# Kernel tuning notes

Measured on AMD Instinct MI355X. Metric: run time of the kernel, lower is better.

## Reference

```python
import jax, jax.numpy as jnp
import numpy as np

N_NODES = 50000
N_EDGES = 800000
D_IN = 128
D_HID = 256
N_CLASSES = 2
N_GRAPHS = 256


def _graph_conv(x, src, dst, W_root, W_rel, b, num_nodes):
    # PyG GraphConv: out_i = W_root @ x_i + W_rel @ sum_{j->i} x_j + b
    agg = jax.ops.segment_sum(x[src], dst, num_segments=num_nodes)  # [N, d_in]
    return x @ W_root.T + agg @ W_rel.T + b


def setup_inputs() -> dict:
    key = jax.random.key(0)
    ks = jax.random.split(key, 12)
    x = jax.random.normal(ks[0], (N_NODES, D_IN), dtype=jnp.float32)
    edge_index = jax.random.randint(ks[1], (2, N_EDGES), 0, N_NODES, dtype=jnp.int64)
    batch = jnp.sort(jax.random.randint(ks[2], (N_NODES,), 0, N_GRAPHS, dtype=jnp.int64))
    s1 = 1.0 / np.sqrt(D_IN)
    s2 = 1.0 / np.sqrt(D_HID)
    W1_root = jax.random.uniform(ks[3], (D_HID, D_IN), minval=-s1, maxval=s1, dtype=jnp.float32)
    W1_rel = jax.random.uniform(ks[4], (D_HID, D_IN), minval=-s1, maxval=s1, dtype=jnp.float32)
    b1 = jax.random.uniform(ks[5], (D_HID,), minval=-s1, maxval=s1, dtype=jnp.float32)
    W2_root = jax.random.uniform(ks[6], (D_HID, D_HID), minval=-s2, maxval=s2, dtype=jnp.float32)
    W2_rel = jax.random.uniform(ks[7], (D_HID, D_HID), minval=-s2, maxval=s2, dtype=jnp.float32)
    b2 = jax.random.uniform(ks[8], (D_HID,), minval=-s2, maxval=s2, dtype=jnp.float32)
    Wfc = jax.random.uniform(ks[9], (N_CLASSES, D_HID), minval=-s2, maxval=s2, dtype=jnp.float32)
    bfc = jax.random.uniform(ks[10], (N_CLASSES,), minval=-s2, maxval=s2, dtype=jnp.float32)
    return {"x": x, "edge_index": edge_index, "batch": batch, "num_graphs": N_GRAPHS,
            "W1_root": W1_root, "W1_rel": W1_rel, "b1": b1,
            "W2_root": W2_root, "W2_rel": W2_rel, "b2": b2,
            "Wfc": Wfc, "bfc": bfc}


def reference(x, edge_index, batch, num_graphs, W1_root, W1_rel, b1, W2_root, W2_rel, b2, Wfc, bfc):
    src, dst = edge_index[0], edge_index[1]
    n = x.shape[0]
    h = jax.nn.relu(_graph_conv(x, src, dst, W1_root, W1_rel, b1, n))
    h = jax.nn.relu(_graph_conv(h, src, dst, W2_root, W2_rel, b2, n))
    # global mean pool over graph segments
    sums = jax.ops.segment_sum(h, batch, num_segments=num_graphs)        # [G, d]
    counts = jax.ops.segment_sum(jnp.ones((n,), h.dtype), batch, num_segments=num_graphs)
    pooled = sums / jnp.maximum(counts, 1.0)[:, None]
    logits = pooled @ Wfc.T + bfc
    return jax.nn.sigmoid(logits)
```

## Files before the change

### kernel.cpp

```cpp
#include <hip/hip_runtime.h>
#include <math.h>

#define D_IN 128
#define D_HID 256
#define N_CLASSES 2
#define N_GRAPHS 256
#define BUCKET 64

typedef __attribute__((ext_vector_type(8))) short short8;
typedef __attribute__((ext_vector_type(4))) float float4v;

__device__ __forceinline__ unsigned short f2bf(float f) {
    union { float f; unsigned int u; } v; v.f = f;
    unsigned int r = v.u + 0x7FFFu + ((v.u >> 16) & 1u);
    return (unsigned short)(r >> 16);
}
__device__ __forceinline__ float bf2f(unsigned short h) {
    union { unsigned int u; float f; } v; v.u = ((unsigned int)h) << 16;
    return v.f;
}

#define GLD_LDS16(gp, lp) __builtin_amdgcn_global_load_lds( \
    (const __attribute__((address_space(1))) void*)(gp),    \
    (__attribute__((address_space(3))) void*)(lp), 16, 0, 0)

__global__ void convert_all_kernel(const float* __restrict__ x,
                                   const float* __restrict__ w1r,
                                   const float* __restrict__ w1a,
                                   const float* __restrict__ w2r,
                                   const float* __restrict__ w2a,
                                   unsigned short* __restrict__ xb,
                                   unsigned short* __restrict__ o1r,
                                   unsigned short* __restrict__ o1a,
                                   unsigned short* __restrict__ o2r,
                                   unsigned short* __restrict__ o2a,
                                   int n4x) {
    int i = blockIdx.x * blockDim.x + threadIdx.x;
    const float* in; unsigned short* out; int off;
    if (i < n4x)                 { in = x;   out = xb;  off = i; }
    else {
        int j = i - n4x;
        if (j < 8192)            { in = w1r; out = o1r; off = j; }
        else if (j < 16384)      { in = w1a; out = o1a; off = j - 8192; }
        else if (j < 32768)      { in = w2r; out = o2r; off = j - 16384; }
        else if (j < 49152)      { in = w2a; out = o2a; off = j - 32768; }
        else return;
    }
    float4 v = ((const float4*)in)[off];
    ushort4 o;
    o.x = f2bf(v.x); o.y = f2bf(v.y); o.z = f2bf(v.z); o.w = f2bf(v.w);
    ((ushort4*)out)[off] = o;
}

__global__ void fill_bucket_kernel(const int* __restrict__ src, const int* __restrict__ dst,
                                   int* __restrict__ cursor, unsigned short* __restrict__ srcs,
                                   int E) {
    int e = blockIdx.x * blockDim.x + threadIdx.x;
    if (e < E) {
        int d = dst[e];
        int pos = atomicAdd(&cursor[d], 1);
        if (pos < BUCKET) srcs[d * BUCKET + pos] = (unsigned short)src[e];
    }
}

template <int D>
__global__ void gather_bucket_bf16(const unsigned short* __restrict__ feat,
                                   const unsigned short* __restrict__ srcs,
                                   const int* __restrict__ cnt,
                                   unsigned short* __restrict__ agg, int N) {
    const int wave = (blockIdx.x * blockDim.x + threadIdx.x) >> 6;
    const int lane = threadIdx.x & 63;
    if (wave >= N) return;
    const unsigned short* bucket = srcs + (size_t)wave * BUCKET;
    int my = bucket[lane];
    const int c = min(cnt[wave], BUCKET);

    if (D == 256) {
        float a0 = 0.f, a1 = 0.f, a2 = 0.f, a3 = 0.f;
        float b0 = 0.f, b1 = 0.f, b2 = 0.f, b3 = 0.f;
        const unsigned short* base = feat + lane * 4;
        int i = 0;
        for (; i + 4 <= c; i += 4) {
            int s0 = __shfl(my, i + 0);
            int s1 = __shfl(my, i + 1);
            int s2 = __shfl(my, i + 2);
            int s3 = __shfl(my, i + 3);
            uint2 w0 = *(const uint2*)(base + (size_t)s0 * 256);
            uint2 w1 = *(const uint2*)(base + (size_t)s1 * 256);
            uint2 w2 = *(const uint2*)(base + (size_t)s2 * 256);
            uint2 w3 = *(const uint2*)(base + (size_t)s3 * 256);
            a0 += bf2f((unsigned short)(w0.x & 0xFFFF)); a1 += bf2f((unsigned short)(w0.x >> 16));
            a2 += bf2f((unsigned short)(w0.y & 0xFFFF)); a3 += bf2f((unsigned short)(w0.y >> 16));
            b0 += bf2f((unsigned short)(w1.x & 0xFFFF)); b1 += bf2f((unsigned short)(w1.x >> 16));
            b2 += bf2f((unsigned short)(w1.y & 0xFFFF)); b3 += bf2f((unsigned short)(w1.y >> 16));
            a0 += bf2f((unsigned short)(w2.x & 0xFFFF)); a1 += bf2f((unsigned short)(w2.x >> 16));
            a2 += bf2f((unsigned short)(w2.y & 0xFFFF)); a3 += bf2f((unsigned short)(w2.y >> 16));
            b0 += bf2f((unsigned short)(w3.x & 0xFFFF)); b1 += bf2f((unsigned short)(w3.x >> 16));
            b2 += bf2f((unsigned short)(w3.y & 0xFFFF)); b3 += bf2f((unsigned short)(w3.y >> 16));
        }
        for (; i < c; i++) {
            int s = __shfl(my, i);
            uint2 w = *(const uint2*)(base + (size_t)s * 256);
            a0 += bf2f((unsigned short)(w.x & 0xFFFF)); a1 += bf2f((unsigned short)(w.x >> 16));
            a2 += bf2f((unsigned short)(w.y & 0xFFFF)); a3 += bf2f((unsigned short)(w.y >> 16));
        }
        a0 += b0; a1 += b1; a2 += b2; a3 += b3;
        uint2 o;
        o.x = (unsigned int)f2bf(a0) | ((unsigned int)f2bf(a1) << 16);
        o.y = (unsigned int)f2bf(a2) | ((unsigned int)f2bf(a3) << 16);
        *(uint2*)(agg + (size_t)wave * 256 + lane * 4) = o;
    } else {
        const int half = lane >> 5;
        const int hl = lane & 31;
        float a0 = 0.f, a1 = 0.f, a2 = 0.f, a3 = 0.f;
        float b0 = 0.f, b1 = 0.f, b2 = 0.f, b3 = 0.f;
        const unsigned short* base = feat + hl * 4;
        int i = 0;
        for (; i + 4 <= c; i += 4) {
            int sA = __shfl(my, i + half);
            int sB = __shfl(my, i + 2 + half);
            uint2 wA = *(const uint2*)(base + (size_t)sA * 128);
            uint2 wB = *(const uint2*)(base + (size_t)sB * 128);
            a0 += bf2f((unsigned short)(wA.x & 0xFFFF)); a1 += bf2f((unsigned short)(wA.x >> 16));
            a2 += bf2f((unsigned short)(wA.y & 0xFFFF)); a3 += bf2f((unsigned short)(wA.y >> 16));
            b0 += bf2f((unsigned short)(wB.x & 0xFFFF)); b1 += bf2f((unsigned short)(wB.x >> 16));
            b2 += bf2f((unsigned short)(wB.y & 0xFFFF)); b3 += bf2f((unsigned short)(wB.y >> 16));
        }
        for (; i < c; i += 2) {
            if (i + half < c) {
                int s = __shfl(my, i + half);
                uint2 w = *(const uint2*)(base + (size_t)s * 128);
                a0 += bf2f((unsigned short)(w.x & 0xFFFF)); a1 += bf2f((unsigned short)(w.x >> 16));
                a2 += bf2f((unsigned short)(w.y & 0xFFFF)); a3 += bf2f((unsigned short)(w.y >> 16));
            }
        }
        a0 += b0; a1 += b1; a2 += b2; a3 += b3;
        a0 += __shfl_xor(a0, 32);
        a1 += __shfl_xor(a1, 32);
        a2 += __shfl_xor(a2, 32);
        a3 += __shfl_xor(a3, 32);
        if (half == 0) {
            uint2 o;
            o.x = (unsigned int)f2bf(a0) | ((unsigned int)f2bf(a1) << 16);
            o.y = (unsigned int)f2bf(a2) | ((unsigned int)f2bf(a3) << 16);
            *(uint2*)(agg + (size_t)wave * 128 + hl * 4) = o;
        }
    }
}

template <int K1>
__global__ void gemm_mfma_dual(const unsigned short* __restrict__ X,
                               const unsigned short* __restrict__ Ag,
                               const unsigned short* __restrict__ Wr,
                               const unsigned short* __restrict__ Wa,
                               const float* __restrict__ bias,
                               unsigned short* __restrict__ out,
                               int Nrows) {
    __shared__ __align__(16) unsigned short As[128][32];
    __shared__ __align__(16) unsigned short Bs[128][32];

    const int tid = threadIdx.x;
    const int w = tid >> 6;
    const int lane = tid & 63;
    const int quad = lane >> 4;
    const int r16 = lane & 15;
    const int srow = lane >> 2;
    const int scol = (lane & 3) * 8;
    const int i0 = blockIdx.x * 128;
    const int o0 = blockIdx.y * 128;
    const int m0 = (w >> 1) * 64;
    const int n0 = (w & 1) * 64;

    float4v acc[4][4];
#pragma unroll
    for (int mt = 0; mt < 4; mt++)
#pragma unroll
        for (int nt = 0; nt < 4; nt++) {
            float4v z = {0.f, 0.f, 0.f, 0.f};
            acc[mt][nt] = z;
        }

    for (int k0 = 0; k0 < 2 * K1; k0 += 32) {
        const bool first = (k0 < K1);
        const int kb = first ? k0 : (k0 - K1);
        const unsigned short* PA = first ? X : Ag;
        const unsigned short* PB = first ? Wr : Wa;

#pragma unroll
        for (int t = 0; t < 2; t++) {
            const int rr = w * 32 + t * 16;
            GLD_LDS16(PA + (size_t)(i0 + rr + srow) * K1 + kb + scol, &As[rr][0]);
            GLD_LDS16(PB + (size_t)(o0 + rr + srow) * K1 + kb + scol, &Bs[rr][0]);
        }
        __syncthreads();

        short8 af[4], bfr[4];
#pragma unroll
        for (int mt = 0; mt < 4; mt++)
            af[mt] = *(const short8*)&As[m0 + mt * 16 + r16][quad * 8];
#pragma unroll
        for (int nt = 0; nt < 4; nt++)
            bfr[nt] = *(const short8*)&Bs[n0 + nt * 16 + r16][quad * 8];
#pragma unroll
        for (int mt = 0; mt < 4; mt++)
#pragma unroll
            for (int nt = 0; nt < 4; nt++)
                acc[mt][nt] = __builtin_amdgcn_mfma_f32_16x16x32_bf16(
                    af[mt], bfr[nt], acc[mt][nt], 0, 0, 0);
        __syncthreads();
    }

#pragma unroll
    for (int mt = 0; mt < 4; mt++) {
#pragma unroll
        for (int e = 0; e < 4; e++) {
            const int m = i0 + m0 + mt * 16 + quad * 4 + e;
            if (m >= Nrows) continue;
#pragma unroll
            for (int nt = 0; nt < 4; nt++) {
                const int n = o0 + n0 + nt * 16 + r16;
                float v = acc[mt][nt][e] + bias[n];
                out[(size_t)m * 256 + n] = f2bf(fmaxf(v, 0.f));
            }
        }
    }
}

__global__ void pool_fc_kernel(const unsigned short* __restrict__ h,
                               const int* __restrict__ batch,
                               const float* __restrict__ Wfc,
                               const float* __restrict__ bfc,
                               float* __restrict__ out,
                               int N) {
    const int g = blockIdx.x;
    const int tid = threadIdx.x;
    const int wv = tid >> 6;
    const int lane = tid & 63;

    int lo = 0, hi = N;
    while (lo < hi) { int mid = (lo + hi) >> 1; if (batch[mid] < g) lo = mid + 1; else hi = mid; }
    const int start = lo;
    hi = N;
    while (lo < hi) { int mid = (lo + hi) >> 1; if (batch[mid] < g + 1) lo = mid + 1; else hi = mid; }
    const int end = lo;

    float a0 = 0.f, a1 = 0.f, a2 = 0.f, a3 = 0.f;
    float b0 = 0.f, b1 = 0.f, b2 = 0.f, b3 = 0.f;
    const unsigned short* base = h + lane * 4;
    int r = start + wv;
    for (; r + 16 < end; r += 32) {
        uint2 wA = *(const uint2*)(base + (size_t)r * 256);
        uint2 wB = *(const uint2*)(base + (size_t)(r + 16) * 256);
        a0 += bf2f((unsigned short)(wA.x & 0xFFFF)); a1 += bf2f((unsigned short)(wA.x >> 16));
        a2 += bf2f((unsigned short)(wA.y & 0xFFFF)); a3 += bf2f((unsigned short)(wA.y >> 16));
        b0 += bf2f((unsigned short)(wB.x & 0xFFFF)); b1 += bf2f((unsigned short)(wB.x >> 16));
        b2 += bf2f((unsigned short)(wB.y & 0xFFFF)); b3 += bf2f((unsigned short)(wB.y >> 16));
    }
    if (r < end) {
        uint2 wA = *(const uint2*)(base + (size_t)r * 256);
        a0 += bf2f((unsigned short)(wA.x & 0xFFFF)); a1 += bf2f((unsigned short)(wA.x >> 16));
        a2 += bf2f((unsigned short)(wA.y & 0xFFFF)); a3 += bf2f((unsigned short)(wA.y >> 16));
    }
    a0 += b0; a1 += b1; a2 += b2; a3 += b3;

    __shared__ float part[16][D_HID];
    part[wv][lane * 4 + 0] = a0;
    part[wv][lane * 4 + 1] = a1;
    part[wv][lane * 4 + 2] = a2;
    part[wv][lane * 4 + 3] = a3;
    __syncthreads();

    __shared__ float pooled[D_HID];
    __shared__ float red[2 * D_HID];
    if (tid < D_HID) {
        float s = 0.f;
#pragma unroll
        for (int w2 = 0; w2 < 16; w2++) s += part[w2][tid];
        const float cnt = fmaxf((float)(end - start), 1.0f);
        pooled[tid] = s / cnt;
    }
    __syncthreads();

    if (tid < 2 * D_HID) {
        const int c = tid >> 8;
        const int col = tid & 255;
        red[tid] = pooled[col] * Wfc[c * D_HID + col];
    }
    __syncthreads();
    for (int off = D_HID / 2; off > 0; off >>= 1) {
        if (tid < 2 * D_HID && (tid & 255) < off) red[tid] += red[tid + off];
        __syncthreads();
    }
    if (tid < N_CLASSES) {
        float logit = red[tid << 8] + bfc[tid];
        out[g * N_CLASSES + tid] = 1.0f / (1.0f + expf(-logit));
    }
}

extern "C" void kernel_launch(void* const* d_in, const int* in_sizes, int n_in,
                              void* d_out, int out_size, void* d_ws, size_t ws_size,
                              hipStream_t stream) {
    const float* x     = (const float*)d_in[0];
    const int*   edge  = (const int*)d_in[1];
    const int*   batch = (const int*)d_in[2];
    const float* W1r = (const float*)d_in[4];
    const float* W1a = (const float*)d_in[5];
    const float* b1  = (const float*)d_in[6];
    const float* W2r = (const float*)d_in[7];
    const float* W2a = (const float*)d_in[8];
    const float* b2  = (const float*)d_in[9];
    const float* Wfc = (const float*)d_in[10];
    const float* bfc = (const float*)d_in[11];

    const int N = in_sizes[0] / D_IN;
    const int E = in_sizes[1] / 2;
    const int* src = edge;
    const int* dst = edge + E;

    unsigned short* xb    = (unsigned short*)d_ws;
    unsigned short* agg1b = xb    + (size_t)N * 128;
    unsigned short* h1b   = agg1b + (size_t)N * 128;
    unsigned short* agg2b = h1b   + (size_t)N * 256;
    unsigned short* h2b   = agg2b + (size_t)N * 256;
    unsigned short* w1r_b = h2b   + (size_t)N * 256;
    unsigned short* w1a_b = w1r_b + 256 * 128;
    unsigned short* w2r_b = w1a_b + 256 * 128;
    unsigned short* w2a_b = w2r_b + 256 * 256;
    int* cursor = (int*)(w2a_b + 256 * 256);
    unsigned short* srcs = (unsigned short*)(cursor + N);

    hipMemsetAsync(cursor, 0, (size_t)N * sizeof(int), stream);

    {
        int n4x = N * D_IN / 4;
        int total = n4x + 49152;
        convert_all_kernel<<<(total + 255) / 256, 256, 0, stream>>>(
            x, W1r, W1a, W2r, W2a, xb, w1r_b, w1a_b, w2r_b, w2a_b, n4x);
    }

    fill_bucket_kernel<<<(E + 255) / 256, 256, 0, stream>>>(src, dst, cursor, srcs, E);

    gather_bucket_bf16<D_IN><<<(N + 3) / 4, 256, 0, stream>>>(xb, srcs, cursor, agg1b, N);
    {
        dim3 grid((N + 127) / 128, 2);
        gemm_mfma_dual<D_IN><<<grid, 256, 0, stream>>>(
            xb, agg1b, w1r_b, w1a_b, b1, h1b, N);
    }

    gather_bucket_bf16<D_HID><<<(N + 3) / 4, 256, 0, stream>>>(h1b, srcs, cursor, agg2b, N);
    {
        dim3 grid((N + 127) / 128, 2);
        gemm_mfma_dual<D_HID><<<grid, 256, 0, stream>>>(
            h1b, agg2b, w2r_b, w2a_b, b2, h2b, N);
    }

    pool_fc_kernel<<<N_GRAPHS, 1024, 0, stream>>>(h2b, batch, Wfc, bfc, (float*)d_out, N);
}
```

Before: 280.3 us.

## Pad neighbor buckets to multiples of 8 with a zero row, fuse convert and fill

```diff
diff --git a/kernel.cpp b/kernel.cpp
--- a/kernel.cpp
+++ b/kernel.cpp
@@ -19,48 +19,73 @@
     union { unsigned int u; float f; } v; v.u = ((unsigned int)h) << 16;
     return v.f;
 }
+__device__ __forceinline__ float blo(unsigned int u) {
+    union { unsigned int u; float f; } v; v.u = u << 16; return v.f;
+}
+__device__ __forceinline__ float bhi(unsigned int u) {
+    union { unsigned int u; float f; } v; v.u = u & 0xFFFF0000u; return v.f;
+}
 
 #define GLD_LDS16(gp, lp) __builtin_amdgcn_global_load_lds( \
     (const __attribute__((address_space(1))) void*)(gp),    \
     (__attribute__((address_space(3))) void*)(lp), 16, 0, 0)
 
-__global__ void convert_all_kernel(const float* __restrict__ x,
-                                   const float* __restrict__ w1r,
-                                   const float* __restrict__ w1a,
-                                   const float* __restrict__ w2r,
-                                   const float* __restrict__ w2a,
-                                   unsigned short* __restrict__ xb,
-                                   unsigned short* __restrict__ o1r,
-                                   unsigned short* __restrict__ o1a,
-                                   unsigned short* __restrict__ o2r,
-                                   unsigned short* __restrict__ o2a,
-                                   int n4x) {
-    int i = blockIdx.x * blockDim.x + threadIdx.x;
-    const float* in; unsigned short* out; int off;
-    if (i < n4x)                 { in = x;   out = xb;  off = i; }
-    else {
-        int j = i - n4x;
-        if (j < 8192)            { in = w1r; out = o1r; off = j; }
-        else if (j < 16384)      { in = w1a; out = o1a; off = j - 8192; }
-        else if (j < 32768)      { in = w2r; out = o2r; off = j - 16384; }
-        else if (j < 49152)      { in = w2a; out = o2a; off = j - 32768; }
-        else return;
-    }
-    float4 v = ((const float4*)in)[off];
-    ushort4 o;
-    o.x = f2bf(v.x); o.y = f2bf(v.y); o.z = f2bf(v.z); o.w = f2bf(v.w);
-    ((ushort4*)out)[off] = o;
-}
-
-__global__ void fill_bucket_kernel(const int* __restrict__ src, const int* __restrict__ dst,
-                                   int* __restrict__ cursor, unsigned short* __restrict__ srcs,
-                                   int E) {
-    int e = blockIdx.x * blockDim.x + threadIdx.x;
-    if (e < E) {
-        int d = dst[e];
-        int pos = atomicAdd(&cursor[d], 1);
-        if (pos < BUCKET) srcs[d * BUCKET + pos] = (unsigned short)src[e];
-    }
+__global__ void convert_fill_kernel(const float* __restrict__ x,
+                                    const float* __restrict__ w1r,
+                                    const float* __restrict__ w1a,
+                                    const float* __restrict__ w2r,
+                                    const float* __restrict__ w2a,
+                                    unsigned short* __restrict__ xb,
+                                    unsigned short* __restrict__ o1r,
+                                    unsigned short* __restrict__ o1a,
+                                    unsigned short* __restrict__ o2r,
+                                    unsigned short* __restrict__ o2a,
+                                    int n4x,
+                                    const int* __restrict__ src,
+                                    const int* __restrict__ dst,
+                                    int* __restrict__ cursor,
+                                    unsigned short* __restrict__ srcs,
+                                    int E, int convBlocks) {
+    if ((int)blockIdx.x < convBlocks) {
+        int i = blockIdx.x * blockDim.x + threadIdx.x;
+        const float* in; unsigned short* out; int off;
+        if (i < n4x)            { in = x;   out = xb;  off = i; }
+        else {
+            int j = i - n4x;
+            if (j < 8192)       { in = w1r; out = o1r; off = j; }
+            else if (j < 16384) { in = w1a; out = o1a; off = j - 8192; }
+            else if (j < 32768) { in = w2r; out = o2r; off = j - 16384; }
+            else if (j < 49152) { in = w2a; out = o2a; off = j - 32768; }
+            else return;
+        }
+        float4 v = ((const float4*)in)[off];
+        ushort4 o;
+        o.x = f2bf(v.x); o.y = f2bf(v.y); o.z = f2bf(v.z); o.w = f2bf(v.w);
+        ((ushort4*)out)[off] = o;
+    } else {
+        int e = ((int)blockIdx.x - convBlocks) * blockDim.x + threadIdx.x;
+        if (e < E) {
+            int d = dst[e];
+            int pos = atomicAdd(&cursor[d], 1);
+            if (pos < BUCKET) srcs[d * BUCKET + pos] = (unsigned short)src[e];
+        }
+    }
+}
+
+__global__ void pad_bucket_kernel(const int* __restrict__ cursor,
+                                  unsigned short* __restrict__ srcs,
+                                  unsigned short* __restrict__ xb_rowN,
+                                  unsigned short* __restrict__ h1b_rowN,
+                                  int N) {
+    if (blockIdx.x == 0) {
+        if (threadIdx.x < 64)  ((unsigned int*)xb_rowN)[threadIdx.x] = 0;
+        if (threadIdx.x < 128) ((unsigned int*)h1b_rowN)[threadIdx.x] = 0;
+    }
+    int n = blockIdx.x * blockDim.x + threadIdx.x;
+    if (n >= N) return;
+    int c = min(cursor[n], BUCKET);
+    int cpad = (c + 7) & ~7;
+    for (int i = c; i < cpad; i++) srcs[n * BUCKET + i] = (unsigned short)N;
 }
 
 template <int D>
@@ -74,35 +99,37 @@
     const unsigned short* bucket = srcs + (size_t)wave * BUCKET;
     int my = bucket[lane];
     const int c = min(cnt[wave], BUCKET);
+    const int cpad = (c + 7) & ~7;
 
     if (D == 256) {
         float a0 = 0.f, a1 = 0.f, a2 = 0.f, a3 = 0.f;
         float b0 = 0.f, b1 = 0.f, b2 = 0.f, b3 = 0.f;
         const unsigned short* base = feat + lane * 4;
-        int i = 0;
-        for (; i + 4 <= c; i += 4) {
+        for (int i = 0; i < cpad; i += 8) {
             int s0 = __shfl(my, i + 0);
             int s1 = __shfl(my, i + 1);
             int s2 = __shfl(my, i + 2);
             int s3 = __shfl(my, i + 3);
+            int s4 = __shfl(my, i + 4);
+            int s5 = __shfl(my, i + 5);
+            int s6 = __shfl(my, i + 6);
+            int s7 = __shfl(my, i + 7);
             uint2 w0 = *(const uint2*)(base + (size_t)s0 * 256);
             uint2 w1 = *(const uint2*)(base + (size_t)s1 * 256);
             uint2 w2 = *(const uint2*)(base + (size_t)s2 * 256);
             uint2 w3 = *(const uint2*)(base + (size_t)s3 * 256);
-            a0 += bf2f((unsigned short)(w0.x & 0xFFFF)); a1 += bf2f((unsigned short)(w0.x >> 16));
-            a2 += bf2f((unsigned short)(w0.y & 0xFFFF)); a3 += bf2f((unsigned short)(w0.y >> 16));
-            b0 += bf2f((unsigned short)(w1.x & 0xFFFF)); b1 += bf2f((unsigned short)(w1.x >> 16));
-            b2 += bf2f((unsigned short)(w1.y & 0xFFFF)); b3 += bf2f((unsigned short)(w1.y >> 16));
-            a0 += bf2f((unsigned short)(w2.x & 0xFFFF)); a1 += bf2f((unsigned short)(w2.x >> 16));
-            a2 += bf2f((unsigned short)(w2.y & 0xFFFF)); a3 += bf2f((unsigned short)(w2.y >> 16));
-            b0 += bf2f((unsigned short)(w3.x & 0xFFFF)); b1 += bf2f((unsigned short)(w3.x >> 16));
-            b2 += bf2f((unsigned short)(w3.y & 0xFFFF)); b3 += bf2f((unsigned short)(w3.y >> 16));
-        }
-        for (; i < c; i++) {
-            int s = __shfl(my, i);
-            uint2 w = *(const uint2*)(base + (size_t)s * 256);
-            a0 += bf2f((unsigned short)(w.x & 0xFFFF)); a1 += bf2f((unsigned short)(w.x >> 16));
-            a2 += bf2f((unsigned short)(w.y & 0xFFFF)); a3 += bf2f((unsigned short)(w.y >> 16));
+            uint2 w4 = *(const uint2*)(base + (size_t)s4 * 256);
+            uint2 w5 = *(const uint2*)(base + (size_t)s5 * 256);
+            uint2 w6 = *(const uint2*)(base + (size_t)s6 * 256);
+            uint2 w7 = *(const uint2*)(base + (size_t)s7 * 256);
+            a0 += blo(w0.x); a1 += bhi(w0.x); a2 += blo(w0.y); a3 += bhi(w0.y);
+            b0 += blo(w1.x); b1 += bhi(w1.x); b2 += blo(w1.y); b3 += bhi(w1.y);
+            a0 += blo(w2.x); a1 += bhi(w2.x); a2 += blo(w2.y); a3 += bhi(w2.y);
+            b0 += blo(w3.x); b1 += bhi(w3.x); b2 += blo(w3.y); b3 += bhi(w3.y);
+            a0 += blo(w4.x); a1 += bhi(w4.x); a2 += blo(w4.y); a3 += bhi(w4.y);
+            b0 += blo(w5.x); b1 += bhi(w5.x); b2 += blo(w5.y); b3 += bhi(w5.y);
+            a0 += blo(w6.x); a1 += bhi(w6.x); a2 += blo(w6.y); a3 += bhi(w6.y);
+            b0 += blo(w7.x); b1 += bhi(w7.x); b2 += blo(w7.y); b3 += bhi(w7.y);
         }
         a0 += b0; a1 += b1; a2 += b2; a3 += b3;
         uint2 o;
@@ -115,24 +142,19 @@
         float a0 = 0.f, a1 = 0.f, a2 = 0.f, a3 = 0.f;
         float b0 = 0.f, b1 = 0.f, b2 = 0.f, b3 = 0.f;
         const unsigned short* base = feat + hl * 4;
-        int i = 0;
-        for (; i + 4 <= c; i += 4) {
-            int sA = __shfl(my, i + half);
+        for (int i = 0; i < cpad; i += 8) {
+            int sA = __shfl(my, i + 0 + half);
             int sB = __shfl(my, i + 2 + half);
+            int sC = __shfl(my, i + 4 + half);
+            int sD = __shfl(my, i + 6 + half);
             uint2 wA = *(const uint2*)(base + (size_t)sA * 128);
             uint2 wB = *(const uint2*)(base + (size_t)sB * 128);
-            a0 += bf2f((unsigned short)(wA.x & 0xFFFF)); a1 += bf2f((unsigned short)(wA.x >> 16));
-            a2 += bf2f((unsigned short)(wA.y & 0xFFFF)); a3 += bf2f((unsigned short)(wA.y >> 16));
-            b0 += bf2f((unsigned short)(wB.x & 0xFFFF)); b1 += bf2f((unsigned short)(wB.x >> 16));
-            b2 += bf2f((unsigned short)(wB.y & 0xFFFF)); b3 += bf2f((unsigned short)(wB.y >> 16));
-        }
-        for (; i < c; i += 2) {
-            if (i + half < c) {
-                int s = __shfl(my, i + half);
-                uint2 w = *(const uint2*)(base + (size_t)s * 128);
-                a0 += bf2f((unsigned short)(w.x & 0xFFFF)); a1 += bf2f((unsigned short)(w.x >> 16));
-                a2 += bf2f((unsigned short)(w.y & 0xFFFF)); a3 += bf2f((unsigned short)(w.y >> 16));
-            }
+            uint2 wC = *(const uint2*)(base + (size_t)sC * 128);
+            uint2 wD = *(const uint2*)(base + (size_t)sD * 128);
+            a0 += blo(wA.x); a1 += bhi(wA.x); a2 += blo(wA.y); a3 += bhi(wA.y);
+            b0 += blo(wB.x); b1 += bhi(wB.x); b2 += blo(wB.y); b3 += bhi(wB.y);
+            a0 += blo(wC.x); a1 += bhi(wC.x); a2 += blo(wC.y); a3 += bhi(wC.y);
+            b0 += blo(wD.x); b1 += bhi(wD.x); b2 += blo(wD.y); b3 += bhi(wD.y);
         }
         a0 += b0; a1 += b1; a2 += b2; a3 += b3;
         a0 += __shfl_xor(a0, 32);
@@ -251,15 +273,12 @@
     for (; r + 16 < end; r += 32) {
         uint2 wA = *(const uint2*)(base + (size_t)r * 256);
         uint2 wB = *(const uint2*)(base + (size_t)(r + 16) * 256);
-        a0 += bf2f((unsigned short)(wA.x & 0xFFFF)); a1 += bf2f((unsigned short)(wA.x >> 16));
-        a2 += bf2f((unsigned short)(wA.y & 0xFFFF)); a3 += bf2f((unsigned short)(wA.y >> 16));
-        b0 += bf2f((unsigned short)(wB.x & 0xFFFF)); b1 += bf2f((unsigned short)(wB.x >> 16));
-        b2 += bf2f((unsigned short)(wB.y & 0xFFFF)); b3 += bf2f((unsigned short)(wB.y >> 16));
+        a0 += blo(wA.x); a1 += bhi(wA.x); a2 += blo(wA.y); a3 += bhi(wA.y);
+        b0 += blo(wB.x); b1 += bhi(wB.x); b2 += blo(wB.y); b3 += bhi(wB.y);
     }
     if (r < end) {
         uint2 wA = *(const uint2*)(base + (size_t)r * 256);
-        a0 += bf2f((unsigned short)(wA.x & 0xFFFF)); a1 += bf2f((unsigned short)(wA.x >> 16));
-        a2 += bf2f((unsigned short)(wA.y & 0xFFFF)); a3 += bf2f((unsigned short)(wA.y >> 16));
+        a0 += blo(wA.x); a1 += bhi(wA.x); a2 += blo(wA.y); a3 += bhi(wA.y);
     }
     a0 += b0; a1 += b1; a2 += b2; a3 += b3;
 
@@ -318,9 +337,9 @@
     const int* dst = edge + E;
 
     unsigned short* xb    = (unsigned short*)d_ws;
-    unsigned short* agg1b = xb    + (size_t)N * 128;
+    unsigned short* agg1b = xb    + (size_t)(N + 1) * 128;
     unsigned short* h1b   = agg1b + (size_t)N * 128;
-    unsigned short* agg2b = h1b   + (size_t)N * 256;
+    unsigned short* agg2b = h1b   + (size_t)(N + 1) * 256;
     unsigned short* h2b   = agg2b + (size_t)N * 256;
     unsigned short* w1r_b = h2b   + (size_t)N * 256;
     unsigned short* w1a_b = w1r_b + 256 * 128;
@@ -333,12 +352,15 @@
 
     {
         int n4x = N * D_IN / 4;
-        int total = n4x + 49152;
-        convert_all_kernel<<<(total + 255) / 256, 256, 0, stream>>>(
-            x, W1r, W1a, W2r, W2a, xb, w1r_b, w1a_b, w2r_b, w2a_b, n4x);
-    }
-
-    fill_bucket_kernel<<<(E + 255) / 256, 256, 0, stream>>>(src, dst, cursor, srcs, E);
+        int convBlocks = (n4x + 49152 + 255) / 256;
+        int fillBlocks = (E + 255) / 256;
+        convert_fill_kernel<<<convBlocks + fillBlocks, 256, 0, stream>>>(
+            x, W1r, W1a, W2r, W2a, xb, w1r_b, w1a_b, w2r_b, w2a_b,
+            n4x, src, dst, cursor, srcs, E, convBlocks);
+    }
+
+    pad_bucket_kernel<<<(N + 255) / 256, 256, 0, stream>>>(
+        cursor, srcs, xb + (size_t)N * 128, h1b + (size_t)N * 256, N);
 
     gather_bucket_bf16<D_IN><<<(N + 3) / 4, 256, 0, stream>>>(xb, srcs, cursor, agg1b, N);
     {
```

Result: slower. 297.2 us (+6.0%).
